# Kernel optimization log

Hardware: AMD Instinct MI355X
Metric: run time of the kernel (lower is better)

Reference implementation:

```python
import jax, jax.numpy as jnp
import numpy as np

H = 3584          # hidden_size
NH = 28           # num query heads
NKV = 4           # num kv heads
HD = H // NH      # head_dim = 128
I = 18944         # intermediate_size
EPS = 1e-6
THETA = 1000000.0


def setup_inputs() -> dict:
    key = jax.random.key(0)
    ks = jax.random.split(key, 16)
    B, S = 1, 2048
    s = 0.02
    inp = {
        "hidden_states": jax.random.normal(ks[0], (B, S, H), jnp.float32),
        "position_ids": jnp.broadcast_to(jnp.arange(S, dtype=jnp.int32)[None, :], (B, S)),
        "q_w": jax.random.normal(ks[1], (NH * HD, H), jnp.float32) * s,
        "q_b": jax.random.normal(ks[2], (NH * HD,), jnp.float32) * s,
        "k_w": jax.random.normal(ks[3], (NKV * HD, H), jnp.float32) * s,
        "k_b": jax.random.normal(ks[4], (NKV * HD,), jnp.float32) * s,
        "v_w": jax.random.normal(ks[5], (NKV * HD, H), jnp.float32) * s,
        "v_b": jax.random.normal(ks[6], (NKV * HD,), jnp.float32) * s,
        "o_w": jax.random.normal(ks[7], (H, NH * HD), jnp.float32) * s,
        "gate_w": jax.random.normal(ks[8], (I, H), jnp.float32) * s,
        "up_w": jax.random.normal(ks[9], (I, H), jnp.float32) * s,
        "down_w": jax.random.normal(ks[10], (H, I), jnp.float32) * s,
        "ln1_w": jnp.ones((H,), jnp.float32),
        "ln2_w": jnp.ones((H,), jnp.float32),
    }
    return inp


def _rms_norm(x, w):
    var = jnp.mean(jnp.square(x), axis=-1, keepdims=True)
    return x * jax.lax.rsqrt(var + EPS) * w


def _rope_cos_sin(position_ids):
    # inv_freq: [HD/2]
    inv_freq = 1.0 / (THETA ** (jnp.arange(0, HD, 2, dtype=jnp.float32) / HD))
    ang = position_ids.astype(jnp.float32)[..., None] * inv_freq  # [B,S,HD/2]
    emb = jnp.concatenate([ang, ang], axis=-1)                     # [B,S,HD]
    return jnp.cos(emb)[:, None], jnp.sin(emb)[:, None]            # [B,1,S,HD]


def _rotate_half(x):
    x1, x2 = x[..., : HD // 2], x[..., HD // 2 :]
    return jnp.concatenate([-x2, x1], axis=-1)


def _forward(hidden_states, position_ids, q_w, q_b, k_w, k_b, v_w, v_b,
             o_w, gate_w, up_w, down_w, ln1_w, ln2_w):
    B, S, _ = hidden_states.shape
    residual = hidden_states
    x = _rms_norm(hidden_states, ln1_w)

    q = jnp.einsum("bsh,dh->bsd", x, q_w) + q_b   # [B,S,NH*HD]
    k = jnp.einsum("bsh,dh->bsd", x, k_w) + k_b   # [B,S,NKV*HD]
    v = jnp.einsum("bsh,dh->bsd", x, v_w) + v_b

    q = q.reshape(B, S, NH, HD).transpose(0, 2, 1, 3)    # [B,NH,S,HD]
    k = k.reshape(B, S, NKV, HD).transpose(0, 2, 1, 3)   # [B,NKV,S,HD]
    v = v.reshape(B, S, NKV, HD).transpose(0, 2, 1, 3)

    cos, sin = _rope_cos_sin(position_ids)
    q = q * cos + _rotate_half(q) * sin
    k = k * cos + _rotate_half(k) * sin

    # GQA: group query heads per kv head (NH = NKV * G)
    G = NH // NKV
    qg = q.reshape(B, NKV, G, S, HD)
    scores = jnp.einsum("bhgsd,bhtd->bhgst", qg, k) / jnp.sqrt(jnp.float32(HD))
    probs = jax.nn.softmax(scores, axis=-1)               # no causal mask in source
    attn = jnp.einsum("bhgst,bhtd->bhgsd", probs, v)      # [B,NKV,G,S,HD]
    attn = attn.reshape(B, NH, S, HD).transpose(0, 2, 1, 3).reshape(B, S, H)

    attn_out = jnp.einsum("bsd,hd->bsh", attn, o_w)
    hidden = residual + attn_out

    residual = hidden
    x = _rms_norm(hidden, ln2_w)
    gate = jax.nn.silu(jnp.einsum("bsh,ih->bsi", x, gate_w))
    up = jnp.einsum("bsh,ih->bsi", x, up_w)
    mlp = jnp.einsum("bsi,hi->bsh", gate * up, down_w)
    return residual + mlp


def reference(hidden_states, position_ids, q_w, q_b, k_w, k_b, v_w, v_b,
              o_w, gate_w, up_w, down_w, ln1_w, ln2_w):
    return _forward(hidden_states, position_ids, q_w, q_b, k_w, k_b, v_w, v_b,
                    o_w, gate_w, up_w, down_w, ln1_w, ln2_w)
```

## Files before the change

kernel.cpp:

```cpp
#include <hip/hip_runtime.h>
#include <hip/hip_bf16.h>
#include <stdint.h>

#define S_LEN 2048
#define HDIM  3584
#define NHEAD 28
#define NKVH  4
#define HDHD  128
#define IDIM  18944

typedef __attribute__((ext_vector_type(8))) short short8;
typedef __attribute__((ext_vector_type(4))) float floatx4;
typedef __attribute__((ext_vector_type(4))) unsigned int uint4v;

__device__ __forceinline__ unsigned short f2bf(float f) {
  union { float f; unsigned int u; } v; v.f = f;
  unsigned int r = v.u + 0x7fffu + ((v.u >> 16) & 1u);
  return (unsigned short)(r >> 16);
}
__device__ __forceinline__ float bf2f(unsigned short h) {
  union { unsigned int u; float f; } v; v.u = ((unsigned int)h) << 16;
  return v.f;
}
__device__ __forceinline__ unsigned int pk2(float a, float b) {
  __hip_bfloat162 h = __float22bfloat162_rn(make_float2(a, b));
  union { __hip_bfloat162 h; unsigned int u; } c; c.h = h; return c.u;
}

__device__ __forceinline__ void gload_lds16(const void* g, void* l) {
  __builtin_amdgcn_global_load_lds(
      (const __attribute__((address_space(1))) void*)g,
      (__attribute__((address_space(3))) void*)l, 16, 0, 0);
}

__device__ __forceinline__ int xcd_remap(int id, int total) {
  return (id & 7) * (total >> 3) + (id >> 3);
}

__device__ __forceinline__ void store_out(int MODE, void* outp, const void* aux,
                                          size_t oidx, float v) {
  if (MODE == 0) {
    ((float*)outp)[oidx] = v;
  } else if (MODE == 1) {
    ((unsigned short*)outp)[oidx] = f2bf(v);
  } else if (MODE == 2) {
    ((float*)outp)[oidx] = v + ((const float*)aux)[oidx];
  } else {
    float gt = bf2f(((const unsigned short*)aux)[oidx]);
    float sg = gt / (1.f + __expf(-gt));
    ((unsigned short*)outp)[oidx] = f2bf(sg * v);
  }
}

template<int MODE, bool BIAS>
__global__ __launch_bounds__(256, 2)
void gemm_w(const unsigned short* __restrict__ A, int lda,
            const unsigned short* __restrict__ W,
            const float* __restrict__ bias,
            void* __restrict__ outp, int ldo, int col0,
            const void* __restrict__ aux, int K)
{
  const int g  = xcd_remap(blockIdx.x, gridDim.x);
  const int mb = g & 7;
  const int nb = g >> 3;
  const int t  = threadIdx.x;
  const int w  = t >> 6, l = t & 63, lg = l >> 4, lc = l & 15;
  const int wr = w >> 1, wc = w & 1;

  __shared__ __align__(16) unsigned short As[256 * 64];
  __shared__ __align__(16) unsigned short Bs[128 * 64];

  floatx4 acc[8][4] = {};

  const char* Ablk = (const char*)(A + (size_t)mb * 256 * lda);
  const char* Wblk = (const char*)(W + (size_t)nb * 128 * K);

  const int s_row = t >> 3;
  const int s_scb = (((t & 7) ^ ((t >> 3) & 7)) << 4);
  const int r_sw  = (lc & 7) << 4;

  const size_t abytes = (size_t)lda * 2;
  const size_t wbytes = (size_t)K * 2;
  const int nk = K >> 6;

  for (int kt = 0; kt < nk; ++kt) {
    const char* asrc = Ablk + (size_t)kt * 128 + s_scb;
    #pragma unroll
    for (int i = 0; i < 8; ++i)
      gload_lds16(asrc + (size_t)(i * 32 + s_row) * abytes,
                  (char*)As + i * 4096 + t * 16);
    const char* wsrc = Wblk + (size_t)kt * 128 + s_scb;
    #pragma unroll
    for (int i = 0; i < 4; ++i)
      gload_lds16(wsrc + (size_t)(i * 32 + s_row) * wbytes,
                  (char*)Bs + i * 4096 + t * 16);
    __syncthreads();
    #pragma unroll
    for (int kk = 0; kk < 2; ++kk) {
      const int ko = (kk * 64 + lg * 16) ^ r_sw;
      short8 bfr[4];
      #pragma unroll
      for (int n = 0; n < 4; ++n)
        bfr[n] = *(const short8*)((const char*)Bs + (wc*64 + n*16 + lc) * 128 + ko);
      #pragma unroll
      for (int m = 0; m < 8; ++m) {
        short8 af = *(const short8*)((const char*)As + (wr*128 + m*16 + lc) * 128 + ko);
        #pragma unroll
        for (int n = 0; n < 4; ++n)
          acc[m][n] = __builtin_amdgcn_mfma_f32_16x16x32_bf16(af, bfr[n], acc[m][n], 0, 0, 0);
      }
    }
    __syncthreads();
  }

  float bv[4] = {0.f, 0.f, 0.f, 0.f};
  if (BIAS) {
    #pragma unroll
    for (int n = 0; n < 4; ++n) bv[n] = bias[nb*128 + wc*64 + n*16 + lc];
  }
  #pragma unroll
  for (int m = 0; m < 8; ++m) {
    #pragma unroll
    for (int n = 0; n < 4; ++n) {
      const int colg = col0 + nb*128 + wc*64 + n*16 + lc;
      #pragma unroll
      for (int j = 0; j < 4; ++j) {
        const int rowg = mb*256 + wr*128 + m*16 + lg*4 + j;
        store_out(MODE, outp, aux, (size_t)rowg * ldo + colg, acc[m][n][j] + bv[n]);
      }
    }
  }
}

__global__ __launch_bounds__(256)
void cvt_bf16_kernel(const float* __restrict__ in, unsigned short* __restrict__ out, int n8)
{
  int i = blockIdx.x * 256 + threadIdx.x;
  const int stride = gridDim.x * 256;
  for (; i < n8; i += stride) {
    floatx4 a = *(const floatx4*)(in + (size_t)i * 8);
    floatx4 b = *(const floatx4*)(in + (size_t)i * 8 + 4);
    uint4v p;
    p[0] = pk2(a[0], a[1]); p[1] = pk2(a[2], a[3]);
    p[2] = pk2(b[0], b[1]); p[3] = pk2(b[2], b[3]);
    *(uint4v*)(out + (size_t)i * 8) = p;
  }
}

__global__ void pack_bias_kernel(const float* __restrict__ qb, const float* __restrict__ kb,
                                 const float* __restrict__ vb, float* __restrict__ o)
{
  int i = blockIdx.x * 256 + threadIdx.x;
  if (i < 3584) o[i] = qb[i];
  else if (i < 4096) o[i] = kb[i - 3584];
  else if (i < 4608) o[i] = vb[i - 4096];
}

__global__ __launch_bounds__(448)
void rmsnorm_kernel(const float* __restrict__ x, const float* __restrict__ wgt,
                    unsigned short* __restrict__ out)
{
  const int row = blockIdx.x, t = threadIdx.x;
  const float* xp = x + (size_t)row * HDIM + t * 8;
  floatx4 a = *(const floatx4*)xp;
  floatx4 b = *(const floatx4*)(xp + 4);
  float ss = a[0]*a[0]+a[1]*a[1]+a[2]*a[2]+a[3]*a[3]
           + b[0]*b[0]+b[1]*b[1]+b[2]*b[2]+b[3]*b[3];
  #pragma unroll
  for (int mk = 1; mk < 64; mk <<= 1) ss += __shfl_xor(ss, mk, 64);
  __shared__ float wsum[8];
  if ((t & 63) == 0) wsum[t >> 6] = ss;
  __syncthreads();
  float tot = 0.f;
  #pragma unroll
  for (int i = 0; i < 7; ++i) tot += wsum[i];
  const float sc = rsqrtf(tot * (1.f / 3584.f) + 1e-6f);
  const float* wp = wgt + t * 8;
  short8 o;
  #pragma unroll
  for (int e = 0; e < 4; ++e) o[e]   = (short)f2bf(a[e] * sc * wp[e]);
  #pragma unroll
  for (int e = 0; e < 4; ++e) o[4+e] = (short)f2bf(b[e] * sc * wp[4+e]);
  *(short8*)(out + (size_t)row * HDIM + t * 8) = o;
}

__global__ __launch_bounds__(448)
void add_rmsnorm_kernel(const float* __restrict__ x, const float* __restrict__ y,
                        const float* __restrict__ wgt,
                        float* __restrict__ h1, unsigned short* __restrict__ out)
{
  const int row = blockIdx.x, t = threadIdx.x;
  const size_t base = (size_t)row * HDIM + t * 8;
  floatx4 a = *(const floatx4*)(x + base);
  floatx4 b = *(const floatx4*)(x + base + 4);
  floatx4 c = *(const floatx4*)(y + base);
  floatx4 d = *(const floatx4*)(y + base + 4);
  a += c; b += d;
  *(floatx4*)(h1 + base)     = a;
  *(floatx4*)(h1 + base + 4) = b;
  float ss = a[0]*a[0]+a[1]*a[1]+a[2]*a[2]+a[3]*a[3]
           + b[0]*b[0]+b[1]*b[1]+b[2]*b[2]+b[3]*b[3];
  #pragma unroll
  for (int mk = 1; mk < 64; mk <<= 1) ss += __shfl_xor(ss, mk, 64);
  __shared__ float wsum[8];
  if ((t & 63) == 0) wsum[t >> 6] = ss;
  __syncthreads();
  float tot = 0.f;
  #pragma unroll
  for (int i = 0; i < 7; ++i) tot += wsum[i];
  const float sc = rsqrtf(tot * (1.f / 3584.f) + 1e-6f);
  const float* wp = wgt + t * 8;
  short8 o;
  #pragma unroll
  for (int e = 0; e < 4; ++e) o[e]   = (short)f2bf(a[e] * sc * wp[e]);
  #pragma unroll
  for (int e = 0; e < 4; ++e) o[4+e] = (short)f2bf(b[e] * sc * wp[4+e]);
  *(short8*)(out + (size_t)row * HDIM + t * 8) = o;
}

__global__ void rope_table_kernel(const int* __restrict__ pos, float* __restrict__ tab)
{
  int idx = blockIdx.x * 256 + threadIdx.x;
  int s = idx >> 6, d = idx & 63;
  float p = (float)pos[s];
  float inv = expf(-((float)(2 * d) * (1.f / 128.f)) * 13.815510557964274f);
  float ang = p * inv;
  tab[idx] = cosf(ang);
  tab[S_LEN * 64 + idx] = sinf(ang);
}

template<int NHX>
__global__ void rope_apply_kernel(const float* __restrict__ in, const float* __restrict__ tab,
                                  unsigned short* __restrict__ out, int col0)
{
  int idx = blockIdx.x * 256 + threadIdx.x;
  int d = idx & 63;
  int rem = idx >> 6;
  int hh = rem % NHX;
  int s  = rem / NHX;
  const float* ip = in + (size_t)s * 4608 + col0 + hh * HDHD;
  float x1 = ip[d], x2 = ip[64 + d];
  float c  = tab[s * 64 + d];
  float sn = tab[S_LEN * 64 + s * 64 + d];
  unsigned short* op = out + (size_t)s * (NHX * HDHD) + hh * HDHD;
  op[d]      = f2bf(x1 * c - x2 * sn);
  op[64 + d] = f2bf(x2 * c + x1 * sn);
}

__global__ void vtrans_kernel(const float* __restrict__ qkvf, unsigned short* __restrict__ vt)
{
  int idx = blockIdx.x * 256 + threadIdx.x;
  int s = idx & (S_LEN - 1);
  int c = idx >> 11;
  vt[idx] = f2bf(qkvf[(size_t)s * 4608 + 4096 + c]);
}

__global__ __launch_bounds__(256)
void attn_kernel(const unsigned short* __restrict__ Q,
                 const unsigned short* __restrict__ Kr,
                 const unsigned short* __restrict__ Vt,
                 unsigned short* __restrict__ O)
{
  const int g  = xcd_remap(blockIdx.x, gridDim.x);
  const int qb = g & 31;
  const int h  = g >> 5;
  const int kvh = h / 7;
  const int t = threadIdx.x, w = t >> 6, l = t & 63, lg = l >> 4, lc = l & 15;

  __shared__ __align__(16) unsigned short Ks[64 * 128];
  __shared__ __align__(16) unsigned short Vs[128 * 64];
  __shared__ __align__(16) unsigned short Ps[4][16 * 64];

  const int qrow = qb * 64 + w * 16 + lc;
  short8 qf[4];
  {
    const unsigned short* qp = Q + (size_t)qrow * HDIM + h * HDHD + lg * 8;
    #pragma unroll
    for (int kk = 0; kk < 4; ++kk) qf[kk] = *(const short8*)(qp + kk * 32);
  }

  float mrun[4], lrun[4];
  #pragma unroll
  for (int j = 0; j < 4; ++j) { mrun[j] = -1e30f; lrun[j] = 0.f; }
  floatx4 oacc[8] = {};

  const int k_row = t >> 4;
  const int k_scb = (((t & 15) ^ ((t >> 4) & 7)) << 4);
  const int v_row = t >> 3;
  const int v_scb = (((t & 7) ^ ((t >> 3) & 7)) << 4);
  const int r_sw  = (lc & 7) << 4;
  const float scale = 0.08838834764831843f;

  for (int kt = 0; kt < 32; ++kt) {
    #pragma unroll
    for (int i = 0; i < 4; ++i)
      gload_lds16((const char*)Kr + ((size_t)(kt*64 + i*16 + k_row) * 512 + kvh*128) * 2 + k_scb,
                  (char*)Ks + i * 4096 + t * 16);
    #pragma unroll
    for (int i = 0; i < 4; ++i)
      gload_lds16((const char*)Vt + ((size_t)(kvh*128 + i*32 + v_row) * S_LEN) * 2
                      + (size_t)kt * 128 + v_scb,
                  (char*)Vs + i * 4096 + t * 16);
    __syncthreads();

    floatx4 sacc[4] = {};
    #pragma unroll
    for (int kk = 0; kk < 4; ++kk) {
      #pragma unroll
      for (int n = 0; n < 4; ++n) {
        short8 kf = *(const short8*)((const char*)Ks + (n*16 + lc) * 256
                                     + ((kk*64 + lg*16) ^ r_sw));
        sacc[n] = __builtin_amdgcn_mfma_f32_16x16x32_bf16(qf[kk], kf, sacc[n], 0, 0, 0);
      }
    }

    float pv[4][4], mt[4];
    #pragma unroll
    for (int j = 0; j < 4; ++j) {
      float a0 = sacc[0][j]*scale, a1 = sacc[1][j]*scale;
      float a2 = sacc[2][j]*scale, a3 = sacc[3][j]*scale;
      pv[0][j]=a0; pv[1][j]=a1; pv[2][j]=a2; pv[3][j]=a3;
      mt[j] = fmaxf(fmaxf(a0, a1), fmaxf(a2, a3));
    }
    #pragma unroll
    for (int mk = 1; mk < 16; mk <<= 1)
      #pragma unroll
      for (int j = 0; j < 4; ++j)
        mt[j] = fmaxf(mt[j], __shfl_xor(mt[j], mk, 16));

    float corr[4], rs[4];
    #pragma unroll
    for (int j = 0; j < 4; ++j) {
      float mn = fmaxf(mrun[j], mt[j]);
      corr[j] = __expf(mrun[j] - mn);
      mrun[j] = mn;
      rs[j] = 0.f;
    }
    #pragma unroll
    for (int n = 0; n < 4; ++n)
      #pragma unroll
      for (int j = 0; j < 4; ++j) {
        float p = __expf(pv[n][j] - mrun[j]);
        pv[n][j] = p; rs[j] += p;
      }
    #pragma unroll
    for (int mk = 1; mk < 16; mk <<= 1)
      #pragma unroll
      for (int j = 0; j < 4; ++j)
        rs[j] += __shfl_xor(rs[j], mk, 16);
    #pragma unroll
    for (int j = 0; j < 4; ++j) lrun[j] = lrun[j] * corr[j] + rs[j];
    #pragma unroll
    for (int q = 0; q < 8; ++q) {
      oacc[q][0] *= corr[0]; oacc[q][1] *= corr[1];
      oacc[q][2] *= corr[2]; oacc[q][3] *= corr[3];
    }

    char* pw = (char*)Ps[w];
    #pragma unroll
    for (int n = 0; n < 4; ++n)
      #pragma unroll
      for (int j = 0; j < 4; ++j) {
        const int prow = lg*4 + j;
        *(unsigned short*)(pw + prow*128 + ((((n*16 + lc)*2)) ^ ((prow & 7) << 4)))
            = f2bf(pv[n][j]);
      }

    short8 pa[2];
    #pragma unroll
    for (int ks = 0; ks < 2; ++ks)
      pa[ks] = *(const short8*)(pw + lc*128 + ((ks*64 + lg*16) ^ r_sw));
    #pragma unroll
    for (int ks = 0; ks < 2; ++ks)
      #pragma unroll
      for (int q = 0; q < 8; ++q) {
        short8 vf = *(const short8*)((const char*)Vs + (q*16 + lc) * 128
                                     + ((ks*64 + lg*16) ^ r_sw));
        oacc[q] = __builtin_amdgcn_mfma_f32_16x16x32_bf16(pa[ks], vf, oacc[q], 0, 0, 0);
      }
    __syncthreads();
  }

  float invl[4];
  #pragma unroll
  for (int j = 0; j < 4; ++j) invl[j] = 1.f / lrun[j];
  #pragma unroll
  for (int q = 0; q < 8; ++q)
    #pragma unroll
    for (int j = 0; j < 4; ++j) {
      int rowg = qb*64 + w*16 + lg*4 + j;
      int colg = h*HDHD + q*16 + lc;
      O[(size_t)rowg * HDIM + colg] = f2bf(oacc[q][j] * invl[j]);
    }
}

__global__ void sentinel_kernel(float* out, int n) {
  int i = blockIdx.x * 256 + threadIdx.x;
  if (i < n) out[i] = 1.0e6f;
}

extern "C" void kernel_launch(void* const* d_in, const int* in_sizes, int n_in,
                              void* d_out, int out_size, void* d_ws, size_t ws_size,
                              hipStream_t stream)
{
  (void)in_sizes; (void)n_in;
  const float* hidden = (const float*)d_in[0];
  const int*   pos    = (const int*)d_in[1];
  const float* q_w    = (const float*)d_in[2];
  const float* q_b    = (const float*)d_in[3];
  const float* k_w    = (const float*)d_in[4];
  const float* k_b    = (const float*)d_in[5];
  const float* v_w    = (const float*)d_in[6];
  const float* v_b    = (const float*)d_in[7];
  const float* o_w    = (const float*)d_in[8];
  const float* gate_w = (const float*)d_in[9];
  const float* up_w   = (const float*)d_in[10];
  const float* down_w = (const float*)d_in[11];
  const float* ln1    = (const float*)d_in[12];
  const float* ln2    = (const float*)d_in[13];
  float* out = (float*)d_out;
  char* ws = (char*)d_ws;

  unsigned short* XN    = (unsigned short*)(ws + 0);
  float*          QKVF  = (float*)(ws + 14680064);
  unsigned short* QR    = (unsigned short*)(ws + 52428800);
  unsigned short* KR    = (unsigned short*)(ws + 67108864);
  unsigned short* VT    = (unsigned short*)(ws + 69206016);
  float*          ROPET = (float*)(ws + 71303168);
  float*          BQKV  = (float*)(ws + 72351744);
  unsigned short* CTX   = (unsigned short*)(ws + 77594624);
  float*          AO    = (float*)(ws + 92274688);
  unsigned short* GBUF  = (unsigned short*)(ws + 0);
  unsigned short* ACT   = (unsigned short*)(ws + 77594624);
  float*          H1    = (float*)(ws + 155189248);
  unsigned short* XN2   = (unsigned short*)(ws + 184549376);
  unsigned short* WB    = (unsigned short*)(ws + 199229440);
  const size_t NEED_BIG = 199229440 + 135790592;

  if (ws_size < NEED_BIG) {
    sentinel_kernel<<<(out_size + 255) / 256, 256, 0, stream>>>(out, out_size);
    return;
  }

  const int CVG = 2048;

  rope_table_kernel<<<(S_LEN * 64) / 256, 256, 0, stream>>>(pos, ROPET);
  rmsnorm_kernel<<<S_LEN, 448, 0, stream>>>(hidden, ln1, XN);

  pack_bias_kernel<<<18, 256, 0, stream>>>(q_b, k_b, v_b, BQKV);
  cvt_bf16_kernel<<<CVG, 256, 0, stream>>>(q_w, WB,               (3584 * 3584) / 8);
  cvt_bf16_kernel<<<CVG, 256, 0, stream>>>(k_w, WB + 3584 * 3584, (512 * 3584) / 8);
  cvt_bf16_kernel<<<CVG, 256, 0, stream>>>(v_w, WB + 4096 * 3584, (512 * 3584) / 8);

  gemm_w<0, true><<<288, 256, 0, stream>>>(XN, HDIM, WB, BQKV, QKVF, 4608, 0, nullptr, HDIM);

  rope_apply_kernel<28><<<(S_LEN * 28 * 64) / 256, 256, 0, stream>>>(QKVF, ROPET, QR, 0);
  rope_apply_kernel<4><<<(S_LEN * 4 * 64) / 256,  256, 0, stream>>>(QKVF, ROPET, KR, 3584);
  vtrans_kernel<<<(512 * S_LEN) / 256, 256, 0, stream>>>(QKVF, VT);

  cvt_bf16_kernel<<<CVG, 256, 0, stream>>>(o_w, WB, (3584 * 3584) / 8);

  attn_kernel<<<28 * 32, 256, 0, stream>>>(QR, KR, VT, CTX);

  gemm_w<0, false><<<224, 256, 0, stream>>>(CTX, HDIM, WB, nullptr, AO, HDIM, 0, nullptr, HDIM);
  add_rmsnorm_kernel<<<S_LEN, 448, 0, stream>>>(hidden, AO, ln2, H1, XN2);

  cvt_bf16_kernel<<<CVG, 256, 0, stream>>>(gate_w, WB, (IDIM * HDIM) / 8);
  gemm_w<1, false><<<1184, 256, 0, stream>>>(XN2, HDIM, WB, nullptr, GBUF, IDIM, 0, nullptr, HDIM);

  cvt_bf16_kernel<<<CVG, 256, 0, stream>>>(up_w, WB, (IDIM * HDIM) / 8);
  gemm_w<3, false><<<1184, 256, 0, stream>>>(XN2, HDIM, WB, nullptr, ACT, IDIM, 0, GBUF, HDIM);

  cvt_bf16_kernel<<<CVG, 256, 0, stream>>>(down_w, WB, (HDIM * IDIM) / 8);
  gemm_w<2, false><<<224, 256, 0, stream>>>(ACT, IDIM, WB, nullptr, out, HDIM, 0, H1, IDIM);
}
```

Baseline: 1.782 ms.

## Add 128x128-tile GEMM for QKV/O/gate/up and double query rows per attention block

Adds a new gemm_bf kernel using 128x128 output tiles with 4 waves each computing 64x64, in place of the 256x128 gemm_w, and uses it for the QKV, O-projection, gate and up GEMMs with twice as many blocks. The attention kernel now processes 128 query rows per block in two groups of 64, so each loaded K/V tile is reused across twice as many queries and grid size halves. The smaller GEMM tiles aim for better occupancy and load balance but give lower arithmetic intensity per tile. The larger attention blocks raise register pressure.

```diff
diff --git a/kernel.cpp b/kernel.cpp
--- a/kernel.cpp
+++ b/kernel.cpp
@@ -53,6 +53,85 @@
 }
 
 template<int MODE, bool BIAS>
+__global__ __launch_bounds__(256)
+void gemm_bf(const unsigned short* __restrict__ A, int lda,
+             const unsigned short* __restrict__ W,
+             const float* __restrict__ bias,
+             void* __restrict__ outp, int ldo, int col0,
+             const void* __restrict__ aux, int K)
+{
+  const int g  = xcd_remap(blockIdx.x, gridDim.x);
+  const int mb = g & 15;
+  const int nb = g >> 4;
+  const int t = threadIdx.x;
+  const int w = t >> 6, l = t & 63, lg = l >> 4, lc = l & 15;
+  const int wr = w >> 1, wc = w & 1;
+
+  __shared__ __align__(16) unsigned short As[128 * 64];
+  __shared__ __align__(16) unsigned short Ws[128 * 64];
+
+  floatx4 acc[4][4] = {};
+
+  const char* Ablk = (const char*)(A + (size_t)mb * 128 * lda);
+  const char* Wblk = (const char*)(W + (size_t)nb * 128 * K);
+
+  const int s_row = t >> 3;
+  const int s_scb = (((t & 7) ^ ((t >> 3) & 7)) << 4);
+  const int r_sw  = (lc & 7) << 4;
+
+  const size_t abytes = (size_t)lda * 2;
+  const size_t wbytes = (size_t)K * 2;
+  const int nk = K >> 6;
+  for (int kt = 0; kt < nk; ++kt) {
+    #pragma unroll
+    for (int i = 0; i < 4; ++i)
+      gload_lds16(Ablk + (size_t)(i * 32 + s_row) * abytes + (size_t)kt * 128 + s_scb,
+                  (char*)As + i * 4096 + t * 16);
+    #pragma unroll
+    for (int i = 0; i < 4; ++i)
+      gload_lds16(Wblk + (size_t)(i * 32 + s_row) * wbytes + (size_t)kt * 128 + s_scb,
+                  (char*)Ws + i * 4096 + t * 16);
+    __syncthreads();
+    #pragma unroll
+    for (int kk = 0; kk < 2; ++kk) {
+      short8 afr[4], bfr[4];
+      #pragma unroll
+      for (int m = 0; m < 4; ++m)
+        afr[m] = *(const short8*)((const char*)As + (wr*64 + m*16 + lc) * 128
+                                 + ((kk*64 + lg*16) ^ r_sw));
+      #pragma unroll
+      for (int n = 0; n < 4; ++n)
+        bfr[n] = *(const short8*)((const char*)Ws + (wc*64 + n*16 + lc) * 128
+                                  + ((kk*64 + lg*16) ^ r_sw));
+      #pragma unroll
+      for (int m = 0; m < 4; ++m)
+        #pragma unroll
+        for (int n = 0; n < 4; ++n)
+          acc[m][n] = __builtin_amdgcn_mfma_f32_16x16x32_bf16(afr[m], bfr[n], acc[m][n], 0, 0, 0);
+    }
+    __syncthreads();
+  }
+
+  float bv[4] = {0.f, 0.f, 0.f, 0.f};
+  if (BIAS) {
+    #pragma unroll
+    for (int n = 0; n < 4; ++n) bv[n] = bias[nb*128 + wc*64 + n*16 + lc];
+  }
+  #pragma unroll
+  for (int m = 0; m < 4; ++m) {
+    #pragma unroll
+    for (int n = 0; n < 4; ++n) {
+      const int colg = col0 + nb*128 + wc*64 + n*16 + lc;
+      #pragma unroll
+      for (int j = 0; j < 4; ++j) {
+        const int rowg = mb*128 + wr*64 + m*16 + lg*4 + j;
+        store_out(MODE, outp, aux, (size_t)rowg * ldo + colg, acc[m][n][j] + bv[n]);
+      }
+    }
+  }
+}
+
+template<int MODE, bool BIAS>
 __global__ __launch_bounds__(256, 2)
 void gemm_w(const unsigned short* __restrict__ A, int lda,
             const unsigned short* __restrict__ W,
@@ -262,8 +341,8 @@
                  unsigned short* __restrict__ O)
 {
   const int g  = xcd_remap(blockIdx.x, gridDim.x);
-  const int qb = g & 31;
-  const int h  = g >> 5;
+  const int qb = g & 15;
+  const int h  = g >> 4;
   const int kvh = h / 7;
   const int t = threadIdx.x, w = t >> 6, l = t & 63, lg = l >> 4, lc = l & 15;
 
@@ -271,18 +350,21 @@
   __shared__ __align__(16) unsigned short Vs[128 * 64];
   __shared__ __align__(16) unsigned short Ps[4][16 * 64];
 
-  const int qrow = qb * 64 + w * 16 + lc;
-  short8 qf[4];
-  {
+  short8 qf[2][4];
+  #pragma unroll
+  for (int grp = 0; grp < 2; ++grp) {
+    const int qrow = qb * 128 + grp * 64 + w * 16 + lc;
     const unsigned short* qp = Q + (size_t)qrow * HDIM + h * HDHD + lg * 8;
     #pragma unroll
-    for (int kk = 0; kk < 4; ++kk) qf[kk] = *(const short8*)(qp + kk * 32);
-  }
-
-  float mrun[4], lrun[4];
-  #pragma unroll
-  for (int j = 0; j < 4; ++j) { mrun[j] = -1e30f; lrun[j] = 0.f; }
-  floatx4 oacc[8] = {};
+    for (int kk = 0; kk < 4; ++kk) qf[grp][kk] = *(const short8*)(qp + kk * 32);
+  }
+
+  float mrun[2][4], lrun[2][4];
+  #pragma unroll
+  for (int grp = 0; grp < 2; ++grp)
+    #pragma unroll
+    for (int j = 0; j < 4; ++j) { mrun[grp][j] = -1e30f; lrun[grp][j] = 0.f; }
+  floatx4 oacc[2][8] = {};
 
   const int k_row = t >> 4;
   const int k_scb = (((t & 15) ^ ((t >> 4) & 7)) << 4);
@@ -303,95 +385,101 @@
                   (char*)Vs + i * 4096 + t * 16);
     __syncthreads();
 
-    floatx4 sacc[4] = {};
-    #pragma unroll
-    for (int kk = 0; kk < 4; ++kk) {
-      #pragma unroll
-      for (int n = 0; n < 4; ++n) {
-        short8 kf = *(const short8*)((const char*)Ks + (n*16 + lc) * 256
-                                     + ((kk*64 + lg*16) ^ r_sw));
-        sacc[n] = __builtin_amdgcn_mfma_f32_16x16x32_bf16(qf[kk], kf, sacc[n], 0, 0, 0);
-      }
+    #pragma unroll
+    for (int grp = 0; grp < 2; ++grp) {
+      floatx4 sacc[4] = {};
+      #pragma unroll
+      for (int kk = 0; kk < 4; ++kk) {
+        #pragma unroll
+        for (int n = 0; n < 4; ++n) {
+          short8 kf = *(const short8*)((const char*)Ks + (n*16 + lc) * 256
+                                       + ((kk*64 + lg*16) ^ r_sw));
+          sacc[n] = __builtin_amdgcn_mfma_f32_16x16x32_bf16(qf[grp][kk], kf, sacc[n], 0, 0, 0);
+        }
+      }
+
+      float pv[4][4], mt[4];
+      #pragma unroll
+      for (int j = 0; j < 4; ++j) {
+        float a0 = sacc[0][j]*scale, a1 = sacc[1][j]*scale;
+        float a2 = sacc[2][j]*scale, a3 = sacc[3][j]*scale;
+        pv[0][j]=a0; pv[1][j]=a1; pv[2][j]=a2; pv[3][j]=a3;
+        mt[j] = fmaxf(fmaxf(a0, a1), fmaxf(a2, a3));
+      }
+      #pragma unroll
+      for (int mk = 1; mk < 16; mk <<= 1)
+        #pragma unroll
+        for (int j = 0; j < 4; ++j)
+          mt[j] = fmaxf(mt[j], __shfl_xor(mt[j], mk, 16));
+
+      float corr[4], rs[4];
+      #pragma unroll
+      for (int j = 0; j < 4; ++j) {
+        float mn = fmaxf(mrun[grp][j], mt[j]);
+        corr[j] = __expf(mrun[grp][j] - mn);
+        mrun[grp][j] = mn;
+        rs[j] = 0.f;
+      }
+      #pragma unroll
+      for (int n = 0; n < 4; ++n)
+        #pragma unroll
+        for (int j = 0; j < 4; ++j) {
+          float p = __expf(pv[n][j] - mrun[grp][j]);
+          pv[n][j] = p; rs[j] += p;
+        }
+      #pragma unroll
+      for (int mk = 1; mk < 16; mk <<= 1)
+        #pragma unroll
+        for (int j = 0; j < 4; ++j)
+          rs[j] += __shfl_xor(rs[j], mk, 16);
+      #pragma unroll
+      for (int j = 0; j < 4; ++j) lrun[grp][j] = lrun[grp][j] * corr[j] + rs[j];
+      #pragma unroll
+      for (int q = 0; q < 8; ++q) {
+        oacc[grp][q][0] *= corr[0]; oacc[grp][q][1] *= corr[1];
+        oacc[grp][q][2] *= corr[2]; oacc[grp][q][3] *= corr[3];
+      }
+
+      char* pw = (char*)Ps[w];
+      #pragma unroll
+      for (int n = 0; n < 4; ++n)
+        #pragma unroll
+        for (int j = 0; j < 4; ++j) {
+          const int prow = lg*4 + j;
+          *(unsigned short*)(pw + prow*128 + ((((n*16 + lc)*2)) ^ ((prow & 7) << 4)))
+              = f2bf(pv[n][j]);
+        }
+
+      short8 pa[2];
+      #pragma unroll
+      for (int ks = 0; ks < 2; ++ks)
+        pa[ks] = *(const short8*)(pw + lc*128 + ((ks*64 + lg*16) ^ r_sw));
+      #pragma unroll
+      for (int ks = 0; ks < 2; ++ks)
+        #pragma unroll
+        for (int q = 0; q < 8; ++q) {
+          short8 vf = *(const short8*)((const char*)Vs + (q*16 + lc) * 128
+                                       + ((ks*64 + lg*16) ^ r_sw));
+          oacc[grp][q] = __builtin_amdgcn_mfma_f32_16x16x32_bf16(pa[ks], vf, oacc[grp][q], 0, 0, 0);
+        }
     }
-
-    float pv[4][4], mt[4];
-    #pragma unroll
-    for (int j = 0; j < 4; ++j) {
-      float a0 = sacc[0][j]*scale, a1 = sacc[1][j]*scale;
-      float a2 = sacc[2][j]*scale, a3 = sacc[3][j]*scale;
-      pv[0][j]=a0; pv[1][j]=a1; pv[2][j]=a2; pv[3][j]=a3;
-      mt[j] = fmaxf(fmaxf(a0, a1), fmaxf(a2, a3));
-    }
-    #pragma unroll
-    for (int mk = 1; mk < 16; mk <<= 1)
-      #pragma unroll
-      for (int j = 0; j < 4; ++j)
-        mt[j] = fmaxf(mt[j], __shfl_xor(mt[j], mk, 16));
-
-    float corr[4], rs[4];
-    #pragma unroll
-    for (int j = 0; j < 4; ++j) {
-      float mn = fmaxf(mrun[j], mt[j]);
-      corr[j] = __expf(mrun[j] - mn);
-      mrun[j] = mn;
-      rs[j] = 0.f;
-    }
-    #pragma unroll
-    for (int n = 0; n < 4; ++n)
+    __syncthreads();
+  }
+
+  #pragma unroll
+  for (int grp = 0; grp < 2; ++grp) {
+    float invl[4];
+    #pragma unroll
+    for (int j = 0; j < 4; ++j) invl[j] = 1.f / lrun[grp][j];
+    #pragma unroll
+    for (int q = 0; q < 8; ++q)
       #pragma unroll
       for (int j = 0; j < 4; ++j) {
-        float p = __expf(pv[n][j] - mrun[j]);
-        pv[n][j] = p; rs[j] += p;
-      }
-    #pragma unroll
-    for (int mk = 1; mk < 16; mk <<= 1)
-      #pragma unroll
-      for (int j = 0; j < 4; ++j)
-        rs[j] += __shfl_xor(rs[j], mk, 16);
-    #pragma unroll
-    for (int j = 0; j < 4; ++j) lrun[j] = lrun[j] * corr[j] + rs[j];
-    #pragma unroll
-    for (int q = 0; q < 8; ++q) {
-      oacc[q][0] *= corr[0]; oacc[q][1] *= corr[1];
-      oacc[q][2] *= corr[2]; oacc[q][3] *= corr[3];
-    }
-
-    char* pw = (char*)Ps[w];
-    #pragma unroll
-    for (int n = 0; n < 4; ++n)
-      #pragma unroll
-      for (int j = 0; j < 4; ++j) {
-        const int prow = lg*4 + j;
-        *(unsigned short*)(pw + prow*128 + ((((n*16 + lc)*2)) ^ ((prow & 7) << 4)))
-            = f2bf(pv[n][j]);
-      }
-
-    short8 pa[2];
-    #pragma unroll
-    for (int ks = 0; ks < 2; ++ks)
-      pa[ks] = *(const short8*)(pw + lc*128 + ((ks*64 + lg*16) ^ r_sw));
-    #pragma unroll
-    for (int ks = 0; ks < 2; ++ks)
-      #pragma unroll
-      for (int q = 0; q < 8; ++q) {
-        short8 vf = *(const short8*)((const char*)Vs + (q*16 + lc) * 128
-                                     + ((ks*64 + lg*16) ^ r_sw));
-        oacc[q] = __builtin_amdgcn_mfma_f32_16x16x32_bf16(pa[ks], vf, oacc[q], 0, 0, 0);
-      }
-    __syncthreads();
-  }
-
-  float invl[4];
-  #pragma unroll
-  for (int j = 0; j < 4; ++j) invl[j] = 1.f / lrun[j];
-  #pragma unroll
-  for (int q = 0; q < 8; ++q)
-    #pragma unroll
-    for (int j = 0; j < 4; ++j) {
-      int rowg = qb*64 + w*16 + lg*4 + j;
-      int colg = h*HDHD + q*16 + lc;
-      O[(size_t)rowg * HDIM + colg] = f2bf(oacc[q][j] * invl[j]);
-    }
+        int rowg = qb*128 + grp*64 + w*16 + lg*4 + j;
+        int colg = h*HDHD + q*16 + lc;
+        O[(size_t)rowg * HDIM + colg] = f2bf(oacc[grp][q][j] * invl[j]);
+      }
+  }
 }
 
 __global__ void sentinel_kernel(float* out, int n) {
@@ -452,7 +540,7 @@
   cvt_bf16_kernel<<<CVG, 256, 0, stream>>>(k_w, WB + 3584 * 3584, (512 * 3584) / 8);
   cvt_bf16_kernel<<<CVG, 256, 0, stream>>>(v_w, WB + 4096 * 3584, (512 * 3584) / 8);
 
-  gemm_w<0, true><<<288, 256, 0, stream>>>(XN, HDIM, WB, BQKV, QKVF, 4608, 0, nullptr, HDIM);
+  gemm_bf<0, true><<<576, 256, 0, stream>>>(XN, HDIM, WB, BQKV, QKVF, 4608, 0, nullptr, HDIM);
 
   rope_apply_kernel<28><<<(S_LEN * 28 * 64) / 256, 256, 0, stream>>>(QKVF, ROPET, QR, 0);
   rope_apply_kernel<4><<<(S_LEN * 4 * 64) / 256,  256, 0, stream>>>(QKVF, ROPET, KR, 3584);
@@ -460,16 +548,16 @@
 
   cvt_bf16_kernel<<<CVG, 256, 0, stream>>>(o_w, WB, (3584 * 3584) / 8);
 
-  attn_kernel<<<28 * 32, 256, 0, stream>>>(QR, KR, VT, CTX);
-
-  gemm_w<0, false><<<224, 256, 0, stream>>>(CTX, HDIM, WB, nullptr, AO, HDIM, 0, nullptr, HDIM);
+  attn_kernel<<<448, 256, 0, stream>>>(QR, KR, VT, CTX);
+
+  gemm_bf<0, false><<<448, 256, 0, stream>>>(CTX, HDIM, WB, nullptr, AO, HDIM, 0, nullptr, HDIM);
   add_rmsnorm_kernel<<<S_LEN, 448, 0, stream>>>(hidden, AO, ln2, H1, XN2);
 
   cvt_bf16_kernel<<<CVG, 256, 0, stream>>>(gate_w, WB, (IDIM * HDIM) / 8);
-  gemm_w<1, false><<<1184, 256, 0, stream>>>(XN2, HDIM, WB, nullptr, GBUF, IDIM, 0, nullptr, HDIM);
+  gemm_bf<1, false><<<2368, 256, 0, stream>>>(XN2, HDIM, WB, nullptr, GBUF, IDIM, 0, nullptr, HDIM);
 
   cvt_bf16_kernel<<<CVG, 256, 0, stream>>>(up_w, WB, (IDIM * HDIM) / 8);
-  gemm_w<3, false><<<1184, 256, 0, stream>>>(XN2, HDIM, WB, nullptr, ACT, IDIM, 0, GBUF, HDIM);
+  gemm_bf<3, false><<<2368, 256, 0, stream>>>(XN2, HDIM, WB, nullptr, ACT, IDIM, 0, GBUF, HDIM);
 
   cvt_bf16_kernel<<<CVG, 256, 0, stream>>>(down_w, WB, (HDIM * IDIM) / 8);
   gemm_w<2, false><<<224, 256, 0, stream>>>(ACT, IDIM, WB, nullptr, out, HDIM, 0, H1, IDIM);
```

Result: slower. 2.009 ms (+12.7%).
